# Optimization experiments

Hardware: AMD Instinct MI355X
Metric: run time of the kernel (lower is better)

Reference implementation:

```python
import jax, jax.numpy as jnp
import numpy as np

B, N, E = 4, 1024, 8192
NF_IN, NF_H, NF_OUT = 32, 128, 3


def _lin(key, fan_in, fan_out):
    k1, k2 = jax.random.split(key)
    bound = 1.0 / np.sqrt(fan_in)
    W = jax.random.uniform(k1, (fan_in, fan_out), jnp.float32, -bound, bound)
    b = jax.random.uniform(k2, (fan_out,), jnp.float32, -bound, bound)
    return W, b


def setup_inputs() -> dict:
    key = jax.random.key(0)
    ks = jax.random.split(key, 16)
    x = jax.random.normal(ks[0], (B, N, NF_IN), jnp.float32)
    # One-hot receiver/sender relation matrices [B, E, N]
    recv = jax.random.randint(ks[1], (B, E), 0, N)
    send = jax.random.randint(ks[2], (B, E), 0, N)
    Rr = jax.nn.one_hot(recv, N, dtype=jnp.float32)
    Rs = jax.nn.one_hot(send, N, dtype=jnp.float32)
    neW0, neb0 = _lin(ks[3], NF_IN, NF_H)
    neW1, neb1 = _lin(ks[4], NF_H, NF_H)
    neW2, neb2 = _lin(ks[5], NF_H, NF_H)
    eeW0, eeb0 = _lin(ks[6], NF_IN * 2, NF_H)
    eeW1, eeb1 = _lin(ks[7], NF_H, NF_H)
    eeW2, eeb2 = _lin(ks[8], NF_H, NF_H)
    npW, npb = _lin(ks[9], NF_H * 2, NF_H)
    epW, epb = _lin(ks[10], NF_H * 3, NF_H)
    ppW0, ppb0 = _lin(ks[11], NF_H * 2, NF_H)
    ppW1, ppb1 = _lin(ks[12], NF_H, NF_H)
    ppW2, ppb2 = _lin(ks[13], NF_H, NF_OUT)
    return dict(x=x, Rr=Rr, Rs=Rs, pstep=2,
                neW0=neW0, neb0=neb0, neW1=neW1, neb1=neb1, neW2=neW2, neb2=neb2,
                eeW0=eeW0, eeb0=eeb0, eeW1=eeW1, eeb1=eeb1, eeW2=eeW2, eeb2=eeb2,
                npW=npW, npb=npb, epW=epW, epb=epb,
                ppW0=ppW0, ppb0=ppb0, ppW1=ppW1, ppb1=ppb1, ppW2=ppW2, ppb2=ppb2)


def _encoder(x, W0, b0, W1, b1, W2, b2):
    # Linear->ReLU x3 (ReLU after last layer too)
    h = jax.nn.relu(x @ W0 + b0)
    h = jax.nn.relu(h @ W1 + b1)
    return jax.nn.relu(h @ W2 + b2)


def _predictor(x, W0, b0, W1, b1, W2, b2):
    h = jax.nn.relu(x @ W0 + b0)
    h = jax.nn.relu(h @ W1 + b1)
    return h @ W2 + b2


def reference(x, Rr, Rs, pstep,
              neW0, neb0, neW1, neb1, neW2, neb2,
              eeW0, eeb0, eeW1, eeb1, eeW2, eeb2,
              npW, npb, epW, epb,
              ppW0, ppb0, ppW1, ppb1, ppW2, ppb2):
    node_encode = _encoder(x, neW0, neb0, neW1, neb1, neW2, neb2)  # [B,N,H]
    node_effect = node_encode
    x_r = jnp.einsum('ben,bnf->bef', Rr, x)  # gather receiver features
    x_s = jnp.einsum('ben,bnf->bef', Rs, x)  # gather sender features
    edge_encode = _encoder(jnp.concatenate([x_r, x_s], -1),
                           eeW0, eeb0, eeW1, eeb1, eeW2, eeb2)  # [B,E,H]
    for _ in range(pstep):
        ne_r = jnp.einsum('ben,bnh->beh', Rr, node_effect)
        ne_s = jnp.einsum('ben,bnh->beh', Rs, node_effect)
        edge_in = jnp.concatenate([edge_encode, ne_r, ne_s], -1)  # [B,E,3H]
        edge_effect = jax.nn.relu(edge_in @ epW + epb)  # [B,E,H]
        agg = jnp.einsum('ben,beh->bnh', Rr, edge_effect)  # scatter-add to receivers
        node_in = jnp.concatenate([node_encode, agg], -1)  # [B,N,2H]
        node_effect = jax.nn.relu(node_in @ npW + npb + node_effect)  # residual
    node_reps = _predictor(jnp.concatenate([node_encode, node_effect], -1),
                           ppW0, ppb0, ppW1, ppb1, ppW2, ppb2)  # [B,N,out]
    return node_reps
```

## Files before the change

### kernel.cpp

```cpp
#include <hip/hip_runtime.h>
#include <hip/hip_bf16.h>


typedef unsigned short u16;
typedef __attribute__((ext_vector_type(8))) __bf16 bf16x8;
typedef __attribute__((ext_vector_type(4))) float f32x4;

#define N_    1024
#define BN    4096
#define BE    32768
#define LOG_E 13
#define H_    128
#define LSTR  132

__device__ __forceinline__ u16 f2bf(float f) {
    __bf16 h = (__bf16)f;
    return __builtin_bit_cast(u16, h);
}

__device__ __forceinline__ bf16x8 cvt8(float4 f0, float4 f1) {
    bf16x8 a;
    a[0] = (__bf16)f0.x; a[1] = (__bf16)f0.y; a[2] = (__bf16)f0.z; a[3] = (__bf16)f0.w;
    a[4] = (__bf16)f1.x; a[5] = (__bf16)f1.y; a[6] = (__bf16)f1.z; a[7] = (__bf16)f1.w;
    return a;
}

__device__ __forceinline__ bf16x8 a_from_f32(const float* p) {
    float4 f0 = *(const float4*)p;
    float4 f1 = *(const float4*)(p + 4);
    return cvt8(f0, f1);
}

__device__ __forceinline__ bf16x8 a_from_lds(const float* lds, int m, int quad, int c) {
    return a_from_f32(lds + m * LSTR + c * 32 + quad * 8);
}

__device__ __forceinline__ void mm8(const u16* __restrict__ Wf, int c, bf16x8 a,
                                    f32x4* acc, int lane) {
    const u16* wp = Wf + ((size_t)c * 8) * 64 * 8;
    #pragma unroll
    for (int nt = 0; nt < 8; ++nt) {
        bf16x8 bw = *(const bf16x8*)(wp + (size_t)(nt * 64 + lane) * 8);
        acc[nt] = __builtin_amdgcn_mfma_f32_16x16x32_bf16(a, bw, acc[nt], 0, 0, 0);
    }
}

__device__ __forceinline__ void zacc(f32x4* acc) {
    #pragma unroll
    for (int t = 0; t < 8; ++t) acc[t] = (f32x4){0.f, 0.f, 0.f, 0.f};
}

__device__ __forceinline__ void epi_to_lds(float* lds, const f32x4* acc,
                                           const float* __restrict__ bias,
                                           int quad, int m) {
    #pragma unroll
    for (int nt = 0; nt < 8; ++nt) {
        float bv = bias[nt * 16 + m];
        #pragma unroll
        for (int i = 0; i < 4; ++i)
            lds[(quad * 4 + i) * LSTR + nt * 16 + m] = fmaxf(acc[nt][i] + bv, 0.f);
    }
}

struct WDesc { const float* src; u16* dst; int K; };
struct WPack { WDesc d[10]; };

__global__ __launch_bounds__(256) void k_wprep(WPack P, float* __restrict__ agg) {
    if (blockIdx.y == 10) {
        int i = blockIdx.x * 256 + threadIdx.x;
        for (int t = i; t < BN * H_ / 4; t += 192 * 256)
            ((float4*)agg)[t] = make_float4(0.f, 0.f, 0.f, 0.f);
        return;
    }
    WDesc d = P.d[blockIdx.y];
    int i = blockIdx.x * 256 + threadIdx.x;
    if (i >= d.K * 128) return;
    int j    = i & 7;
    int lane = (i >> 3) & 63;
    int nt   = (i >> 9) & 7;
    int c    = i >> 12;
    int k = c * 32 + (lane >> 4) * 8 + j;
    int n = nt * 16 + (lane & 15);
    d.dst[i] = f2bf(d.src[k * 128 + n]);
}

__global__ __launch_bounds__(256) void k_extract(const float* __restrict__ Rr,
                                                 const float* __restrict__ Rs,
                                                 int* __restrict__ recv,
                                                 int* __restrict__ send) {
    int wave = threadIdx.x >> 6, lane = threadIdx.x & 63;
    int g = blockIdx.x * 4 + wave;
    const float* src;
    int* dst;
    if (g < BE) { src = Rr + (size_t)g * N_;        dst = recv + g; }
    else        { src = Rs + (size_t)(g - BE) * N_; dst = send + (g - BE); }
    int idx = 0;
    bool done = false;
    #pragma unroll
    for (int it = 0; it < 4; ++it) {
        if (!done) {
            int base = it * 256 + lane * 4;
            float4 v = *(const float4*)(src + base);
            int found = -1;
            if      (v.x != 0.f) found = base;
            else if (v.y != 0.f) found = base + 1;
            else if (v.z != 0.f) found = base + 2;
            else if (v.w != 0.f) found = base + 3;
            unsigned long long msk = __ballot(found >= 0);
            if (msk) {
                int sl = __ffsll((long long)msk) - 1;
                idx = __shfl(found, sl, 64);
                done = true;
            }
        }
    }
    if (lane == 0) *dst = idx;
}

__global__ __launch_bounds__(64) void k_node3(
    const float* __restrict__ x,
    const u16* __restrict__ W0, const float* __restrict__ b0,
    const u16* __restrict__ W1, const float* __restrict__ b1,
    const u16* __restrict__ W2, const float* __restrict__ b2,
    float* __restrict__ nenc)
{
    __shared__ float lds[2][16 * LSTR];
    int lane = threadIdx.x, m = lane & 15, quad = lane >> 4;
    int row16 = blockIdx.x * 16;
    f32x4 acc[8];

    zacc(acc);
    mm8(W0, 0, a_from_f32(x + (size_t)(row16 + m) * 32 + quad * 8), acc, lane);
    epi_to_lds(lds[0], acc, b0, quad, m);

    zacc(acc);
    #pragma unroll
    for (int c = 0; c < 4; ++c) mm8(W1, c, a_from_lds(lds[0], m, quad, c), acc, lane);
    epi_to_lds(lds[1], acc, b1, quad, m);

    zacc(acc);
    #pragma unroll
    for (int c = 0; c < 4; ++c) mm8(W2, c, a_from_lds(lds[1], m, quad, c), acc, lane);
    epi_to_lds(lds[0], acc, b2, quad, m);

    #pragma unroll
    for (int t = 0; t < 32; ++t) {
        int flat = t * 64 + lane;
        int r = flat >> 7, col = flat & 127;
        nenc[(size_t)(row16 + r) * H_ + col] = lds[0][r * LSTR + col];
    }
}

__global__ __launch_bounds__(64) void k_edge3(
    const float* __restrict__ x,
    const int* __restrict__ recv, const int* __restrict__ send,
    const u16* __restrict__ W0, const float* __restrict__ b0,
    const u16* __restrict__ W1, const float* __restrict__ b1,
    const u16* __restrict__ W2, const float* __restrict__ b2,
    u16* __restrict__ eenc)
{
    __shared__ float lds[2][16 * LSTR];
    int lane = threadIdx.x, m = lane & 15, quad = lane >> 4;
    int row16 = blockIdx.x * 16;
    int e = row16 + m, b = e >> LOG_E;
    long rr = (long)b * N_ + recv[e];
    long rs = (long)b * N_ + send[e];
    f32x4 acc[8];

    zacc(acc);
    mm8(W0, 0, a_from_f32(x + rr * 32 + quad * 8), acc, lane);
    mm8(W0, 1, a_from_f32(x + rs * 32 + quad * 8), acc, lane);
    epi_to_lds(lds[0], acc, b0, quad, m);

    zacc(acc);
    #pragma unroll
    for (int c = 0; c < 4; ++c) mm8(W1, c, a_from_lds(lds[0], m, quad, c), acc, lane);
    epi_to_lds(lds[1], acc, b1, quad, m);

    zacc(acc);
    #pragma unroll
    for (int c = 0; c < 4; ++c) mm8(W2, c, a_from_lds(lds[1], m, quad, c), acc, lane);
    epi_to_lds(lds[0], acc, b2, quad, m);

    #pragma unroll
    for (int t = 0; t < 16; ++t) {
        int r = t, col = lane * 2;
        u16 lo = f2bf(lds[0][r * LSTR + col]);
        u16 hi = f2bf(lds[0][r * LSTR + col + 1]);
        *(unsigned*)(eenc + (size_t)(row16 + r) * H_ + col) =
            (unsigned)lo | ((unsigned)hi << 16);
    }
}

__global__ __launch_bounds__(64) void k_eprop(
    const u16* __restrict__ eenc, const float* __restrict__ eff,
    const int* __restrict__ recv, const int* __restrict__ send,
    const u16* __restrict__ Wf, const float* __restrict__ bias,
    float* __restrict__ agg)
{
    int lane = threadIdx.x, m = lane & 15, quad = lane >> 4;
    int row16 = blockIdx.x * 16;
    int e = row16 + m, b = e >> LOG_E;
    long rr = (long)b * N_ + recv[e];
    long rs = (long)b * N_ + send[e];
    f32x4 acc[8];
    zacc(acc);

    #pragma unroll
    for (int c = 0; c < 4; ++c)
        mm8(Wf, c, *(const bf16x8*)(eenc + (size_t)e * H_ + c * 32 + quad * 8), acc, lane);
    #pragma unroll
    for (int c = 0; c < 4; ++c)
        mm8(Wf, 4 + c, a_from_f32(eff + rr * H_ + c * 32 + quad * 8), acc, lane);
    #pragma unroll
    for (int c = 0; c < 4; ++c)
        mm8(Wf, 8 + c, a_from_f32(eff + rs * H_ + c * 32 + quad * 8), acc, lane);

    size_t tgt[4];
    #pragma unroll
    for (int i = 0; i < 4; ++i) {
        int r = row16 + quad * 4 + i;
        tgt[i] = ((size_t)(r >> LOG_E) * N_ + recv[r]) * H_;
    }
    #pragma unroll
    for (int nt = 0; nt < 8; ++nt) {
        int col = nt * 16 + m;
        float bv = bias[col];
        #pragma unroll
        for (int i = 0; i < 4; ++i)
            atomicAdd(agg + tgt[i] + col, fmaxf(acc[nt][i] + bv, 0.f));
    }
}

__global__ __launch_bounds__(64) void k_nprop(
    const float* __restrict__ nenc, float* __restrict__ agg,
    const float* __restrict__ eff,
    const u16* __restrict__ Wf, const float* __restrict__ bias,
    float* __restrict__ nout)
{
    int lane = threadIdx.x, m = lane & 15, quad = lane >> 4;
    int row16 = blockIdx.x * 16;
    int row = row16 + m;
    f32x4 acc[8];
    zacc(acc);

    #pragma unroll
    for (int c = 0; c < 4; ++c)
        mm8(Wf, c, a_from_f32(nenc + (size_t)row * H_ + c * 32 + quad * 8), acc, lane);
    #pragma unroll
    for (int c = 0; c < 4; ++c)
        mm8(Wf, 4 + c, a_from_f32(agg + (size_t)row * H_ + c * 32 + quad * 8), acc, lane);

    #pragma unroll
    for (int nt = 0; nt < 8; ++nt) {
        int col = nt * 16 + m;
        float bv = bias[col];
        #pragma unroll
        for (int i = 0; i < 4; ++i) {
            int r = row16 + quad * 4 + i;
            float v = fmaxf(acc[nt][i] + bv + eff[(size_t)r * H_ + col], 0.f);
            nout[(size_t)r * H_ + col] = v;
            agg[(size_t)r * H_ + col] = 0.f;
        }
    }
}

__global__ __launch_bounds__(64) void k_pred(
    const float* __restrict__ nenc, const float* __restrict__ eff,
    const u16* __restrict__ W0, const float* __restrict__ b0,
    const u16* __restrict__ W1, const float* __restrict__ b1,
    const float* __restrict__ W2, const float* __restrict__ b2,
    float* __restrict__ out)
{
    __shared__ float lds[2][16 * LSTR];
    int lane = threadIdx.x, m = lane & 15, quad = lane >> 4;
    int row16 = blockIdx.x * 16;
    int row = row16 + m;
    f32x4 acc[8];

    zacc(acc);
    #pragma unroll
    for (int c = 0; c < 4; ++c)
        mm8(W0, c, a_from_f32(nenc + (size_t)row * H_ + c * 32 + quad * 8), acc, lane);
    #pragma unroll
    for (int c = 0; c < 4; ++c)
        mm8(W0, 4 + c, a_from_f32(eff + (size_t)row * H_ + c * 32 + quad * 8), acc, lane);
    epi_to_lds(lds[0], acc, b0, quad, m);

    zacc(acc);
    #pragma unroll
    for (int c = 0; c < 4; ++c) mm8(W1, c, a_from_lds(lds[0], m, quad, c), acc, lane);
    epi_to_lds(lds[1], acc, b1, quad, m);

    int r = lane & 15, col = lane >> 4;
    if (col < 3) {
        float s = 0.f;
        #pragma unroll 8
        for (int k = 0; k < 128; ++k)
            s += lds[1][r * LSTR + k] * W2[k * 3 + col];
        out[(size_t)(row16 + r) * 3 + col] = s + b2[col];
    }
}

extern "C" void kernel_launch(void* const* d_in, const int* in_sizes, int n_in,
                              void* d_out, int out_size, void* d_ws, size_t ws_size,
                              hipStream_t stream) {
    (void)in_sizes; (void)n_in; (void)out_size; (void)ws_size;

    const float* x    = (const float*)d_in[0];
    const float* Rr   = (const float*)d_in[1];
    const float* Rs   = (const float*)d_in[2];
    const float* neW0 = (const float*)d_in[4];  const float* neb0 = (const float*)d_in[5];
    const float* neW1 = (const float*)d_in[6];  const float* neb1 = (const float*)d_in[7];
    const float* neW2 = (const float*)d_in[8];  const float* neb2 = (const float*)d_in[9];
    const float* eeW0 = (const float*)d_in[10]; const float* eeb0 = (const float*)d_in[11];
    const float* eeW1 = (const float*)d_in[12]; const float* eeb1 = (const float*)d_in[13];
    const float* eeW2 = (const float*)d_in[14]; const float* eeb2 = (const float*)d_in[15];
    const float* npW  = (const float*)d_in[16]; const float* npb  = (const float*)d_in[17];
    const float* epW  = (const float*)d_in[18]; const float* epb  = (const float*)d_in[19];
    const float* ppW0 = (const float*)d_in[20]; const float* ppb0 = (const float*)d_in[21];
    const float* ppW1 = (const float*)d_in[22]; const float* ppb1 = (const float*)d_in[23];
    const float* ppW2 = (const float*)d_in[24]; const float* ppb2 = (const float*)d_in[25];

    char* ws = (char*)d_ws;
    size_t off = 0;
    auto alloc = [&](size_t bytes) -> char* {
        char* p = ws + off;
        off += (bytes + 255) & ~(size_t)255;
        return p;
    };

    u16* f_neW0 = (u16*)alloc(32  * 128 * 2);
    u16* f_neW1 = (u16*)alloc(128 * 128 * 2);
    u16* f_neW2 = (u16*)alloc(128 * 128 * 2);
    u16* f_eeW0 = (u16*)alloc(64  * 128 * 2);
    u16* f_eeW1 = (u16*)alloc(128 * 128 * 2);
    u16* f_eeW2 = (u16*)alloc(128 * 128 * 2);
    u16* f_epW  = (u16*)alloc(384 * 128 * 2);
    u16* f_npW  = (u16*)alloc(256 * 128 * 2);
    u16* f_ppW0 = (u16*)alloc(256 * 128 * 2);
    u16* f_ppW1 = (u16*)alloc(128 * 128 * 2);
    int*   recv = (int*)alloc(BE * 4);
    int*   send = (int*)alloc(BE * 4);
    float* nenc = (float*)alloc((size_t)BN * H_ * 4);
    float* nef1 = (float*)alloc((size_t)BN * H_ * 4);
    float* nef2 = (float*)alloc((size_t)BN * H_ * 4);
    float* agg  = (float*)alloc((size_t)BN * H_ * 4);
    u16*   eenc = (u16*)alloc((size_t)BE * H_ * 2);

    WPack P;
    P.d[0] = {neW0, f_neW0, 32};
    P.d[1] = {neW1, f_neW1, 128};
    P.d[2] = {neW2, f_neW2, 128};
    P.d[3] = {eeW0, f_eeW0, 64};
    P.d[4] = {eeW1, f_eeW1, 128};
    P.d[5] = {eeW2, f_eeW2, 128};
    P.d[6] = {epW,  f_epW,  384};
    P.d[7] = {npW,  f_npW,  256};
    P.d[8] = {ppW0, f_ppW0, 256};
    P.d[9] = {ppW1, f_ppW1, 128};
    k_wprep<<<dim3(192, 11), 256, 0, stream>>>(P, agg);

    k_extract<<<(2 * BE) / 4, 256, 0, stream>>>(Rr, Rs, recv, send);

    k_node3<<<BN / 16, 64, 0, stream>>>(x, f_neW0, neb0, f_neW1, neb1, f_neW2, neb2, nenc);
    k_edge3<<<BE / 16, 64, 0, stream>>>(x, recv, send,
                                        f_eeW0, eeb0, f_eeW1, eeb1, f_eeW2, eeb2, eenc);

    k_eprop<<<BE / 16, 64, 0, stream>>>(eenc, nenc, recv, send, f_epW, epb, agg);
    k_nprop<<<BN / 16, 64, 0, stream>>>(nenc, agg, nenc, f_npW, npb, nef1);
    k_eprop<<<BE / 16, 64, 0, stream>>>(eenc, nef1, recv, send, f_epW, epb, agg);
    k_nprop<<<BN / 16, 64, 0, stream>>>(nenc, agg, nef1, f_npW, npb, nef2);

    k_pred<<<BN / 16, 64, 0, stream>>>(nenc, nef2, f_ppW0, ppb0, f_ppW1, ppb1,
                                       ppW2, ppb2, (float*)d_out);
}
```

Baseline: 393.9 us.

## Merge prep, encoder and final node/predictor kernels; store LDS slabs as bf16

The weight repack, agg zeroing and one-hot index extraction now run in a single prep kernel. The node and edge encoders now share one launch, split by block index. The last node-propagation step is fused with the predictor MLP, which removes the nef2 round trip through global memory. The intermediate LDS tiles now hold bf16 instead of fp32, which halves LDS traffic and drops the repeated conversions before each MFMA. The aim is to cut kernel-launch gaps and memory traffic, at the cost of rounding intermediates to bf16 one step earlier and giving the merged prep kernel a less regular workload.

```diff
diff --git a/kernel.cpp b/kernel.cpp
--- a/kernel.cpp
+++ b/kernel.cpp
@@ -11,28 +11,27 @@
 #define BE    32768
 #define LOG_E 13
 #define H_    128
-#define LSTR  132
+#define LSTR  136
+#define TOTW  208896
 
 __device__ __forceinline__ u16 f2bf(float f) {
     __bf16 h = (__bf16)f;
     return __builtin_bit_cast(u16, h);
 }
-
-__device__ __forceinline__ bf16x8 cvt8(float4 f0, float4 f1) {
+__device__ __forceinline__ float bf2f(u16 u) {
+    return __uint_as_float(((unsigned)u) << 16);
+}
+
+__device__ __forceinline__ bf16x8 a_from_f32(const float* p) {
+    float4 f0 = *(const float4*)p;
+    float4 f1 = *(const float4*)(p + 4);
     bf16x8 a;
     a[0] = (__bf16)f0.x; a[1] = (__bf16)f0.y; a[2] = (__bf16)f0.z; a[3] = (__bf16)f0.w;
     a[4] = (__bf16)f1.x; a[5] = (__bf16)f1.y; a[6] = (__bf16)f1.z; a[7] = (__bf16)f1.w;
     return a;
 }
-
-__device__ __forceinline__ bf16x8 a_from_f32(const float* p) {
-    float4 f0 = *(const float4*)p;
-    float4 f1 = *(const float4*)(p + 4);
-    return cvt8(f0, f1);
-}
-
-__device__ __forceinline__ bf16x8 a_from_lds(const float* lds, int m, int quad, int c) {
-    return a_from_f32(lds + m * LSTR + c * 32 + quad * 8);
+__device__ __forceinline__ bf16x8 a_from_slab(const u16* s, int m, int quad, int c) {
+    return *(const bf16x8*)(s + m * LSTR + c * 32 + quad * 8);
 }
 
 __device__ __forceinline__ void mm8(const u16* __restrict__ Wf, int c, bf16x8 a,
@@ -44,151 +43,141 @@
         acc[nt] = __builtin_amdgcn_mfma_f32_16x16x32_bf16(a, bw, acc[nt], 0, 0, 0);
     }
 }
-
 __device__ __forceinline__ void zacc(f32x4* acc) {
     #pragma unroll
     for (int t = 0; t < 8; ++t) acc[t] = (f32x4){0.f, 0.f, 0.f, 0.f};
 }
-
-__device__ __forceinline__ void epi_to_lds(float* lds, const f32x4* acc,
-                                           const float* __restrict__ bias,
-                                           int quad, int m) {
+__device__ __forceinline__ void epi_slab(u16* s, const f32x4* acc,
+                                         const float* __restrict__ bias,
+                                         int quad, int m) {
     #pragma unroll
     for (int nt = 0; nt < 8; ++nt) {
         float bv = bias[nt * 16 + m];
         #pragma unroll
         for (int i = 0; i < 4; ++i)
-            lds[(quad * 4 + i) * LSTR + nt * 16 + m] = fmaxf(acc[nt][i] + bv, 0.f);
-    }
-}
-
-struct WDesc { const float* src; u16* dst; int K; };
+            s[(quad * 4 + i) * LSTR + nt * 16 + m] = f2bf(fmaxf(acc[nt][i] + bv, 0.f));
+    }
+}
+
+struct WDesc { const float* src; u16* dst; };
 struct WPack { WDesc d[10]; };
 
-__global__ __launch_bounds__(256) void k_wprep(WPack P, float* __restrict__ agg) {
-    if (blockIdx.y == 10) {
-        int i = blockIdx.x * 256 + threadIdx.x;
-        for (int t = i; t < BN * H_ / 4; t += 192 * 256)
-            ((float4*)agg)[t] = make_float4(0.f, 0.f, 0.f, 0.f);
-        return;
-    }
-    WDesc d = P.d[blockIdx.y];
-    int i = blockIdx.x * 256 + threadIdx.x;
-    if (i >= d.K * 128) return;
-    int j    = i & 7;
-    int lane = (i >> 3) & 63;
-    int nt   = (i >> 9) & 7;
-    int c    = i >> 12;
-    int k = c * 32 + (lane >> 4) * 8 + j;
-    int n = nt * 16 + (lane & 15);
-    d.dst[i] = f2bf(d.src[k * 128 + n]);
-}
-
-__global__ __launch_bounds__(256) void k_extract(const float* __restrict__ Rr,
-                                                 const float* __restrict__ Rs,
-                                                 int* __restrict__ recv,
-                                                 int* __restrict__ send) {
-    int wave = threadIdx.x >> 6, lane = threadIdx.x & 63;
-    int g = blockIdx.x * 4 + wave;
-    const float* src;
-    int* dst;
-    if (g < BE) { src = Rr + (size_t)g * N_;        dst = recv + g; }
-    else        { src = Rs + (size_t)(g - BE) * N_; dst = send + (g - BE); }
-    int idx = 0;
-    bool done = false;
-    #pragma unroll
-    for (int it = 0; it < 4; ++it) {
-        if (!done) {
-            int base = it * 256 + lane * 4;
-            float4 v = *(const float4*)(src + base);
-            int found = -1;
-            if      (v.x != 0.f) found = base;
-            else if (v.y != 0.f) found = base + 1;
-            else if (v.z != 0.f) found = base + 2;
-            else if (v.w != 0.f) found = base + 3;
-            unsigned long long msk = __ballot(found >= 0);
-            if (msk) {
-                int sl = __ffsll((long long)msk) - 1;
-                idx = __shfl(found, sl, 64);
-                done = true;
+__global__ __launch_bounds__(256) void k_prep(WPack P, float* __restrict__ agg,
+                                              const float* __restrict__ Rr,
+                                              const float* __restrict__ Rs,
+                                              int* __restrict__ recv,
+                                              int* __restrict__ send) {
+    const int Kt[10] = {32, 128, 128, 64, 128, 128, 384, 256, 256, 128};
+    int tg = blockIdx.x * 256 + threadIdx.x;
+
+    if (tg < TOTW) {
+        int pref = 0, base = 0, mi = 0;
+        #pragma unroll
+        for (int q = 0; q < 10; ++q) {
+            int nb = pref + Kt[q] * 128;
+            if (tg >= nb) { base = nb; mi = q + 1; }
+            pref = nb;
+        }
+        int i = tg - base;
+        int j = i & 7, ln = (i >> 3) & 63, nt = (i >> 9) & 7, c = i >> 12;
+        int k = c * 32 + (ln >> 4) * 8 + j;
+        int n = nt * 16 + (ln & 15);
+        P.d[mi].dst[i] = f2bf(P.d[mi].src[k * 128 + n]);
+    }
+    if (tg < BN * H_ / 4)
+        ((float4*)agg)[tg] = make_float4(0.f, 0.f, 0.f, 0.f);
+
+    int wid = blockIdx.x * 4 + (threadIdx.x >> 6);
+    int lane = threadIdx.x & 63;
+    for (int r2 = 0; r2 < 8; ++r2) {
+        int gidx = wid * 8 + r2;
+        const float* src; int* dst;
+        if (gidx < BE) { src = Rr + (size_t)gidx * N_;        dst = recv + gidx; }
+        else           { src = Rs + (size_t)(gidx - BE) * N_; dst = send + (gidx - BE); }
+        int idx = 0;
+        bool done = false;
+        #pragma unroll
+        for (int it = 0; it < 4; ++it) {
+            if (!done) {
+                int bp = it * 256 + lane * 4;
+                float4 v = *(const float4*)(src + bp);
+                int found = -1;
+                if      (v.x != 0.f) found = bp;
+                else if (v.y != 0.f) found = bp + 1;
+                else if (v.z != 0.f) found = bp + 2;
+                else if (v.w != 0.f) found = bp + 3;
+                unsigned long long msk = __ballot(found >= 0);
+                if (msk) {
+                    idx = __shfl(found, __ffsll((long long)msk) - 1, 64);
+                    done = true;
+                }
             }
         }
-    }
-    if (lane == 0) *dst = idx;
-}
-
-__global__ __launch_bounds__(64) void k_node3(
-    const float* __restrict__ x,
-    const u16* __restrict__ W0, const float* __restrict__ b0,
-    const u16* __restrict__ W1, const float* __restrict__ b1,
-    const u16* __restrict__ W2, const float* __restrict__ b2,
-    float* __restrict__ nenc)
-{
-    __shared__ float lds[2][16 * LSTR];
-    int lane = threadIdx.x, m = lane & 15, quad = lane >> 4;
-    int row16 = blockIdx.x * 16;
-    f32x4 acc[8];
-
-    zacc(acc);
-    mm8(W0, 0, a_from_f32(x + (size_t)(row16 + m) * 32 + quad * 8), acc, lane);
-    epi_to_lds(lds[0], acc, b0, quad, m);
-
-    zacc(acc);
-    #pragma unroll
-    for (int c = 0; c < 4; ++c) mm8(W1, c, a_from_lds(lds[0], m, quad, c), acc, lane);
-    epi_to_lds(lds[1], acc, b1, quad, m);
-
-    zacc(acc);
-    #pragma unroll
-    for (int c = 0; c < 4; ++c) mm8(W2, c, a_from_lds(lds[1], m, quad, c), acc, lane);
-    epi_to_lds(lds[0], acc, b2, quad, m);
-
-    #pragma unroll
-    for (int t = 0; t < 32; ++t) {
-        int flat = t * 64 + lane;
-        int r = flat >> 7, col = flat & 127;
-        nenc[(size_t)(row16 + r) * H_ + col] = lds[0][r * LSTR + col];
-    }
-}
-
-__global__ __launch_bounds__(64) void k_edge3(
+        if (lane == 0) *dst = idx;
+    }
+}
+
+__global__ __launch_bounds__(64) void k_enc(
     const float* __restrict__ x,
     const int* __restrict__ recv, const int* __restrict__ send,
-    const u16* __restrict__ W0, const float* __restrict__ b0,
-    const u16* __restrict__ W1, const float* __restrict__ b1,
-    const u16* __restrict__ W2, const float* __restrict__ b2,
-    u16* __restrict__ eenc)
+    const u16* __restrict__ neW0, const float* __restrict__ neb0,
+    const u16* __restrict__ neW1, const float* __restrict__ neb1,
+    const u16* __restrict__ neW2, const float* __restrict__ neb2,
+    const u16* __restrict__ eeW0, const float* __restrict__ eeb0,
+    const u16* __restrict__ eeW1, const float* __restrict__ eeb1,
+    const u16* __restrict__ eeW2, const float* __restrict__ eeb2,
+    float* __restrict__ nenc, u16* __restrict__ eenc)
 {
-    __shared__ float lds[2][16 * LSTR];
+    __shared__ u16 sl0[16 * LSTR];
+    __shared__ u16 sl1[16 * LSTR];
     int lane = threadIdx.x, m = lane & 15, quad = lane >> 4;
-    int row16 = blockIdx.x * 16;
-    int e = row16 + m, b = e >> LOG_E;
-    long rr = (long)b * N_ + recv[e];
-    long rs = (long)b * N_ + send[e];
     f32x4 acc[8];
 
-    zacc(acc);
-    mm8(W0, 0, a_from_f32(x + rr * 32 + quad * 8), acc, lane);
-    mm8(W0, 1, a_from_f32(x + rs * 32 + quad * 8), acc, lane);
-    epi_to_lds(lds[0], acc, b0, quad, m);
-
-    zacc(acc);
-    #pragma unroll
-    for (int c = 0; c < 4; ++c) mm8(W1, c, a_from_lds(lds[0], m, quad, c), acc, lane);
-    epi_to_lds(lds[1], acc, b1, quad, m);
-
-    zacc(acc);
-    #pragma unroll
-    for (int c = 0; c < 4; ++c) mm8(W2, c, a_from_lds(lds[1], m, quad, c), acc, lane);
-    epi_to_lds(lds[0], acc, b2, quad, m);
-
-    #pragma unroll
-    for (int t = 0; t < 16; ++t) {
-        int r = t, col = lane * 2;
-        u16 lo = f2bf(lds[0][r * LSTR + col]);
-        u16 hi = f2bf(lds[0][r * LSTR + col + 1]);
-        *(unsigned*)(eenc + (size_t)(row16 + r) * H_ + col) =
-            (unsigned)lo | ((unsigned)hi << 16);
+    if (blockIdx.x < 2048) {
+        int row16 = blockIdx.x * 16;
+        int e = row16 + m, b = e >> LOG_E;
+        long rr = (long)b * N_ + recv[e];
+        long rs = (long)b * N_ + send[e];
+        zacc(acc);
+        mm8(eeW0, 0, a_from_f32(x + rr * 32 + quad * 8), acc, lane);
+        mm8(eeW0, 1, a_from_f32(x + rs * 32 + quad * 8), acc, lane);
+        epi_slab(sl0, acc, eeb0, quad, m);
+        zacc(acc);
+        #pragma unroll
+        for (int c = 0; c < 4; ++c) mm8(eeW1, c, a_from_slab(sl0, m, quad, c), acc, lane);
+        epi_slab(sl1, acc, eeb1, quad, m);
+        zacc(acc);
+        #pragma unroll
+        for (int c = 0; c < 4; ++c) mm8(eeW2, c, a_from_slab(sl1, m, quad, c), acc, lane);
+        epi_slab(sl0, acc, eeb2, quad, m);
+        #pragma unroll
+        for (int t = 0; t < 16; ++t) {
+            int flat = t * 64 + lane;
+            int r = flat >> 6, col2 = (flat & 63) * 2;
+            unsigned v = (unsigned)sl0[r * LSTR + col2] |
+                         ((unsigned)sl0[r * LSTR + col2 + 1] << 16);
+            *(unsigned*)(eenc + (size_t)(row16 + r) * H_ + col2) = v;
+        }
+    } else {
+        int row16 = (blockIdx.x - 2048) * 16;
+        zacc(acc);
+        mm8(neW0, 0, a_from_f32(x + (size_t)(row16 + m) * 32 + quad * 8), acc, lane);
+        epi_slab(sl0, acc, neb0, quad, m);
+        zacc(acc);
+        #pragma unroll
+        for (int c = 0; c < 4; ++c) mm8(neW1, c, a_from_slab(sl0, m, quad, c), acc, lane);
+        epi_slab(sl1, acc, neb1, quad, m);
+        zacc(acc);
+        #pragma unroll
+        for (int c = 0; c < 4; ++c) mm8(neW2, c, a_from_slab(sl1, m, quad, c), acc, lane);
+        #pragma unroll
+        for (int nt = 0; nt < 8; ++nt) {
+            float bv = neb2[nt * 16 + m];
+            #pragma unroll
+            for (int i = 0; i < 4; ++i)
+                nenc[(size_t)(row16 + quad * 4 + i) * H_ + nt * 16 + m] =
+                    fmaxf(acc[nt][i] + bv, 0.f);
+        }
     }
 }
 
@@ -239,18 +228,15 @@
     float* __restrict__ nout)
 {
     int lane = threadIdx.x, m = lane & 15, quad = lane >> 4;
-    int row16 = blockIdx.x * 16;
-    int row = row16 + m;
+    int row16 = blockIdx.x * 16, row = row16 + m;
     f32x4 acc[8];
     zacc(acc);
-
     #pragma unroll
     for (int c = 0; c < 4; ++c)
         mm8(Wf, c, a_from_f32(nenc + (size_t)row * H_ + c * 32 + quad * 8), acc, lane);
     #pragma unroll
     for (int c = 0; c < 4; ++c)
         mm8(Wf, 4 + c, a_from_f32(agg + (size_t)row * H_ + c * 32 + quad * 8), acc, lane);
-
     #pragma unroll
     for (int nt = 0; nt < 8; ++nt) {
         int col = nt * 16 + m;
@@ -265,40 +251,61 @@
     }
 }
 
-__global__ __launch_bounds__(64) void k_pred(
-    const float* __restrict__ nenc, const float* __restrict__ eff,
-    const u16* __restrict__ W0, const float* __restrict__ b0,
-    const u16* __restrict__ W1, const float* __restrict__ b1,
-    const float* __restrict__ W2, const float* __restrict__ b2,
+__global__ __launch_bounds__(64) void k_nprop_pred(
+    const float* __restrict__ nenc, const float* __restrict__ agg,
+    const float* __restrict__ eff,
+    const u16* __restrict__ Wnp, const float* __restrict__ npb,
+    const u16* __restrict__ Wp0, const float* __restrict__ ppb0,
+    const u16* __restrict__ Wp1, const float* __restrict__ ppb1,
+    const float* __restrict__ ppW2, const float* __restrict__ ppb2,
     float* __restrict__ out)
 {
-    __shared__ float lds[2][16 * LSTR];
+    __shared__ u16 sl0[16 * LSTR];
+    __shared__ u16 sl1[16 * LSTR];
     int lane = threadIdx.x, m = lane & 15, quad = lane >> 4;
-    int row16 = blockIdx.x * 16;
-    int row = row16 + m;
+    int row16 = blockIdx.x * 16, row = row16 + m;
     f32x4 acc[8];
 
     zacc(acc);
     #pragma unroll
     for (int c = 0; c < 4; ++c)
-        mm8(W0, c, a_from_f32(nenc + (size_t)row * H_ + c * 32 + quad * 8), acc, lane);
-    #pragma unroll
-    for (int c = 0; c < 4; ++c)
-        mm8(W0, 4 + c, a_from_f32(eff + (size_t)row * H_ + c * 32 + quad * 8), acc, lane);
-    epi_to_lds(lds[0], acc, b0, quad, m);
-
-    zacc(acc);
-    #pragma unroll
-    for (int c = 0; c < 4; ++c) mm8(W1, c, a_from_lds(lds[0], m, quad, c), acc, lane);
-    epi_to_lds(lds[1], acc, b1, quad, m);
+        mm8(Wnp, c, a_from_f32(nenc + (size_t)row * H_ + c * 32 + quad * 8), acc, lane);
+    #pragma unroll
+    for (int c = 0; c < 4; ++c)
+        mm8(Wnp, 4 + c, a_from_f32(agg + (size_t)row * H_ + c * 32 + quad * 8), acc, lane);
+    #pragma unroll
+    for (int nt = 0; nt < 8; ++nt) {
+        int col = nt * 16 + m;
+        float bv = npb[col];
+        #pragma unroll
+        for (int i = 0; i < 4; ++i) {
+            int r = row16 + quad * 4 + i;
+            float v = fmaxf(acc[nt][i] + bv + eff[(size_t)r * H_ + col], 0.f);
+            sl0[(quad * 4 + i) * LSTR + col] = f2bf(v);
+        }
+    }
+
+    zacc(acc);
+    #pragma unroll
+    for (int c = 0; c < 4; ++c)
+        mm8(Wp0, c, a_from_f32(nenc + (size_t)row * H_ + c * 32 + quad * 8), acc, lane);
+    #pragma unroll
+    for (int c = 0; c < 4; ++c)
+        mm8(Wp0, 4 + c, a_from_slab(sl0, m, quad, c), acc, lane);
+    epi_slab(sl1, acc, ppb0, quad, m);
+
+    zacc(acc);
+    #pragma unroll
+    for (int c = 0; c < 4; ++c) mm8(Wp1, c, a_from_slab(sl1, m, quad, c), acc, lane);
+    epi_slab(sl0, acc, ppb1, quad, m);
 
     int r = lane & 15, col = lane >> 4;
     if (col < 3) {
         float s = 0.f;
         #pragma unroll 8
         for (int k = 0; k < 128; ++k)
-            s += lds[1][r * LSTR + k] * W2[k * 3 + col];
-        out[(size_t)(row16 + r) * 3 + col] = s + b2[col];
+            s += bf2f(sl0[r * LSTR + k]) * ppW2[k * 3 + col];
+        out[(size_t)(row16 + r) * 3 + col] = s + ppb2[col];
     }
 }
 
@@ -307,20 +314,21 @@
                               hipStream_t stream) {
     (void)in_sizes; (void)n_in; (void)out_size; (void)ws_size;
 
-    const float* x    = (const float*)d_in[0];
-    const float* Rr   = (const float*)d_in[1];
-    const float* Rs   = (const float*)d_in[2];
-    const float* neW0 = (const float*)d_in[4];  const float* neb0 = (const float*)d_in[5];
-    const float* neW1 = (const float*)d_in[6];  const float* neb1 = (const float*)d_in[7];
-    const float* neW2 = (const float*)d_in[8];  const float* neb2 = (const float*)d_in[9];
-    const float* eeW0 = (const float*)d_in[10]; const float* eeb0 = (const float*)d_in[11];
-    const float* eeW1 = (const float*)d_in[12]; const float* eeb1 = (const float*)d_in[13];
-    const float* eeW2 = (const float*)d_in[14]; const float* eeb2 = (const float*)d_in[15];
-    const float* npW  = (const float*)d_in[16]; const float* npb  = (const float*)d_in[17];
-    const float* epW  = (const float*)d_in[18]; const float* epb  = (const float*)d_in[19];
-    const float* ppW0 = (const float*)d_in[20]; const float* ppb0 = (const float*)d_in[21];
-    const float* ppW1 = (const float*)d_in[22]; const float* ppb1 = (const float*)d_in[23];
-    const float* ppW2 = (const float*)d_in[24]; const float* ppb2 = (const float*)d_in[25];
+    const float* x  = (const float*)d_in[0];
+    const float* Rr = (const float*)d_in[1];
+    const float* Rs = (const float*)d_in[2];
+    const float* neb0 = (const float*)d_in[5];
+    const float* neb1 = (const float*)d_in[7];
+    const float* neb2 = (const float*)d_in[9];
+    const float* eeb0 = (const float*)d_in[11];
+    const float* eeb1 = (const float*)d_in[13];
+    const float* eeb2 = (const float*)d_in[15];
+    const float* npb  = (const float*)d_in[17];
+    const float* epb  = (const float*)d_in[19];
+    const float* ppb0 = (const float*)d_in[21];
+    const float* ppb1 = (const float*)d_in[23];
+    const float* ppW2 = (const float*)d_in[24];
+    const float* ppb2 = (const float*)d_in[25];
 
     char* ws = (char*)d_ws;
     size_t off = 0;
@@ -330,48 +338,32 @@
         return p;
     };
 
-    u16* f_neW0 = (u16*)alloc(32  * 128 * 2);
-    u16* f_neW1 = (u16*)alloc(128 * 128 * 2);
-    u16* f_neW2 = (u16*)alloc(128 * 128 * 2);
-    u16* f_eeW0 = (u16*)alloc(64  * 128 * 2);
-    u16* f_eeW1 = (u16*)alloc(128 * 128 * 2);
-    u16* f_eeW2 = (u16*)alloc(128 * 128 * 2);
-    u16* f_epW  = (u16*)alloc(384 * 128 * 2);
-    u16* f_npW  = (u16*)alloc(256 * 128 * 2);
-    u16* f_ppW0 = (u16*)alloc(256 * 128 * 2);
-    u16* f_ppW1 = (u16*)alloc(128 * 128 * 2);
+    const int widx[10] = {4, 6, 8, 10, 12, 14, 18, 16, 20, 22};
+    const int Kt[10]   = {32, 128, 128, 64, 128, 128, 384, 256, 256, 128};
+    WPack P;
+    u16* wf[10];
+    for (int i = 0; i < 10; ++i) {
+        wf[i] = (u16*)alloc((size_t)Kt[i] * 128 * 2);
+        P.d[i] = { (const float*)d_in[widx[i]], wf[i] };
+    }
     int*   recv = (int*)alloc(BE * 4);
     int*   send = (int*)alloc(BE * 4);
     float* nenc = (float*)alloc((size_t)BN * H_ * 4);
     float* nef1 = (float*)alloc((size_t)BN * H_ * 4);
-    float* nef2 = (float*)alloc((size_t)BN * H_ * 4);
     float* agg  = (float*)alloc((size_t)BN * H_ * 4);
     u16*   eenc = (u16*)alloc((size_t)BE * H_ * 2);
 
-    WPack P;
-    P.d[0] = {neW0, f_neW0, 32};
-    P.d[1] = {neW1, f_neW1, 128};
-    P.d[2] = {neW2, f_neW2, 128};
-    P.d[3] = {eeW0, f_eeW0, 64};
-    P.d[4] = {eeW1, f_eeW1, 128};
-    P.d[5] = {eeW2, f_eeW2, 128};
-    P.d[6] = {epW,  f_epW,  384};
-    P.d[7] = {npW,  f_npW,  256};
-    P.d[8] = {ppW0, f_ppW0, 256};
-    P.d[9] = {ppW1, f_ppW1, 128};
-    k_wprep<<<dim3(192, 11), 256, 0, stream>>>(P, agg);
-
-    k_extract<<<(2 * BE) / 4, 256, 0, stream>>>(Rr, Rs, recv, send);
-
-    k_node3<<<BN / 16, 64, 0, stream>>>(x, f_neW0, neb0, f_neW1, neb1, f_neW2, neb2, nenc);
-    k_edge3<<<BE / 16, 64, 0, stream>>>(x, recv, send,
-                                        f_eeW0, eeb0, f_eeW1, eeb1, f_eeW2, eeb2, eenc);
-
-    k_eprop<<<BE / 16, 64, 0, stream>>>(eenc, nenc, recv, send, f_epW, epb, agg);
-    k_nprop<<<BN / 16, 64, 0, stream>>>(nenc, agg, nenc, f_npW, npb, nef1);
-    k_eprop<<<BE / 16, 64, 0, stream>>>(eenc, nef1, recv, send, f_epW, epb, agg);
-    k_nprop<<<BN / 16, 64, 0, stream>>>(nenc, agg, nef1, f_npW, npb, nef2);
-
-    k_pred<<<BN / 16, 64, 0, stream>>>(nenc, nef2, f_ppW0, ppb0, f_ppW1, ppb1,
-                                       ppW2, ppb2, (float*)d_out);
-}
+    k_prep<<<2048, 256, 0, stream>>>(P, agg, Rr, Rs, recv, send);
+
+    k_enc<<<2304, 64, 0, stream>>>(x, recv, send,
+                                   wf[0], neb0, wf[1], neb1, wf[2], neb2,
+                                   wf[3], eeb0, wf[4], eeb1, wf[5], eeb2,
+                                   nenc, eenc);
+
+    k_eprop<<<2048, 64, 0, stream>>>(eenc, nenc, recv, send, wf[6], epb, agg);
+    k_nprop<<<256, 64, 0, stream>>>(nenc, agg, nenc, wf[7], npb, nef1);
+    k_eprop<<<2048, 64, 0, stream>>>(eenc, nef1, recv, send, wf[6], epb, agg);
+    k_nprop_pred<<<256, 64, 0, stream>>>(nenc, agg, nef1,
+                                         wf[7], npb, wf[8], ppb0, wf[9], ppb1,
+                                         ppW2, ppb2, (float*)d_out);
+}
```

After: 425.2 us. 1.08x slower.
